# Kernel tuning notes

Measured on AMD Instinct MI355X. Metric: run time of the kernel, lower is better.

Reference implementation:

```python
import jax, jax.numpy as jnp
import numpy as np

T = 8          # time steps (init kwarg T)
GAMA = 1.0     # ZIF surrogate width (init kwarg gama)
LR = 0.1       # adaptive-threshold learning rate (init kwarg learning_rate)
THRESH = 8.0   # init kwarg thresh

# ZIF spiking activation: heaviside forward, triangular surrogate backward
@jax.custom_vjp
def heaviside(u):
    return (u >= 0).astype(u.dtype)

def _hv_fwd(u):
    return (u >= 0).astype(u.dtype), u

def _hv_bwd(u, g):
    surr = (1.0 / GAMA) * (1.0 / GAMA) * jnp.maximum(GAMA - jnp.abs(u), 0.0)
    return (g * surr,)

heaviside.defvjp(_hv_fwd, _hv_bwd)


def setup_inputs() -> dict:
    key = jax.random.key(0)
    x = jax.random.normal(key, (T * 32, 128, 32, 32), dtype=jnp.float32)  # [T*B, C, H, W]
    thresh = jnp.full((1,), THRESH, dtype=jnp.float32)                    # learnable thresh param
    return {"x": x, "thresh": thresh}


def reference(x, thresh):
    # thresh is used via .data in torch -> detached
    thre = jax.lax.stop_gradient(thresh)[0]
    B = x.shape[0] // T
    xs = x.reshape((T, B) + x.shape[1:])           # [T, B, C, H, W]
    C = xs.shape[2]
    neuron_thre0 = jnp.full((C,), thre, x.dtype)   # per-channel threshold init
    cur = neuron_thre0.reshape(1, C, 1, 1)         # broadcasts over [B, C, H, W]

    # sequential IF recurrence over T, carrying membrane potential
    def step(mem, xt):
        mem = mem + xt
        s = heaviside(mem - cur)
        mem = mem - s * cur
        return mem, s

    mem0 = jnp.broadcast_to(0.5 * cur, xs.shape[1:]).astype(x.dtype)
    mem, spikes = jax.lax.scan(step, mem0, xs)     # spikes: [T, B, C, H, W]

    # compensation pass over the stacked spike history
    compen_mem = mem - 0.5 * cur
    spike_count = spikes.sum(axis=0)               # [B, C, H, W]
    compen_value = jnp.minimum(compen_mem + spike_count * cur, T * cur)
    pos = (compen_value > 0) & (spike_count > 0)
    safe_count = jnp.where(spike_count > 0, spike_count, jnp.ones_like(spike_count))
    new_thre = jnp.where(pos, compen_value / safe_count, jnp.zeros_like(compen_value))

    # adaptive threshold update (scalar gradient-descent style step)
    ub = new_thre.mean(axis=(0, 2, 3))             # [C] per-channel target
    diff = ub - neuron_thre0
    mask = jax.lax.stop_gradient((neuron_thre0 > ub).astype(x.dtype))
    update = LR * 2.0 * (diff * mask).mean()       # scalar
    neuron_thre = neuron_thre0 + update            # [C]

    # scale spikes by the updated per-channel threshold, merge temporal dim
    out = spikes * neuron_thre.reshape(1, 1, C, 1, 1)
    return out.reshape((T * B,) + x.shape[1:])
```

## Files before the change

kernel.cpp:

```cpp
#include <hip/hip_runtime.h>
#include <stdint.h>

static constexpr int   T_  = 8;
static constexpr int   C_  = 128;
static constexpr int   N_  = 32 * 128 * 32 * 32;
static constexpr float LR_ = 0.1f;

template <bool PACK>
__global__ __launch_bounds__(256) void k_fwd(const float* __restrict__ x,
                                             const float* __restrict__ thresh,
                                             uint8_t* __restrict__ spk,
                                             float* __restrict__ ub_sum) {
    const float thre = thresh[0];
    const int e4   = blockIdx.x * 256 + threadIdx.x;
    const int base = e4 * 4;

    float    mem[4];
    int      cnt[4] = {0, 0, 0, 0};
    unsigned pb[4]  = {0, 0, 0, 0};
#pragma unroll
    for (int i = 0; i < 4; ++i) mem[i] = 0.5f * thre;

#pragma unroll
    for (int t = 0; t < T_; ++t) {
        const float4 xv = *reinterpret_cast<const float4*>(x + (size_t)t * N_ + base);
        const float xa[4] = {xv.x, xv.y, xv.z, xv.w};
#pragma unroll
        for (int i = 0; i < 4; ++i) {
            mem[i] += xa[i];
            if (mem[i] - thre >= 0.0f) {
                mem[i] -= thre;
                pb[i] |= (1u << t);
                cnt[i]++;
            }
        }
    }

    if (PACK) {
        reinterpret_cast<uchar4*>(spk)[e4] =
            make_uchar4((uint8_t)pb[0], (uint8_t)pb[1], (uint8_t)pb[2], (uint8_t)pb[3]);
    }

    float local = 0.0f;
#pragma unroll
    for (int i = 0; i < 4; ++i) {
        const float compen_mem = mem[i] - 0.5f * thre;
        const float cv = fminf(compen_mem + (float)cnt[i] * thre, (float)T_ * thre);
        if (cv > 0.0f && cnt[i] > 0) local += cv / (float)cnt[i];
    }

#pragma unroll
    for (int off = 32; off > 0; off >>= 1) local += __shfl_down(local, off, 64);
    __shared__ float wpart[4];
    const int lane = threadIdx.x & 63;
    const int wid  = threadIdx.x >> 6;
    if (lane == 0) wpart[wid] = local;
    __syncthreads();
    if (threadIdx.x == 0) {
        const float tot = wpart[0] + wpart[1] + wpart[2] + wpart[3];
        const int c = blockIdx.x & (C_ - 1);
        atomicAdd(ub_sum + c, tot);
    }
}

__global__ __launch_bounds__(128) void k_scalar(const float* __restrict__ ub_sum,
                                                const float* __restrict__ thresh,
                                                float* __restrict__ scal) {
    const float thre = thresh[0];
    const float ub   = ub_sum[threadIdx.x] * (1.0f / 32768.0f);
    float v = (thre > ub) ? (ub - thre) : 0.0f;
#pragma unroll
    for (int off = 32; off > 0; off >>= 1) v += __shfl_down(v, off, 64);
    __shared__ float part[2];
    if ((threadIdx.x & 63) == 0) part[threadIdx.x >> 6] = v;
    __syncthreads();
    if (threadIdx.x == 0) {
        const float update = LR_ * 2.0f * (part[0] + part[1]) * (1.0f / 128.0f);
        scal[0] = thre + update;
    }
}

__global__ __launch_bounds__(256) void k_out(const uint8_t* __restrict__ spk,
                                             const float* __restrict__ scal,
                                             float* __restrict__ out) {
    const int e4   = blockIdx.x * 256 + threadIdx.x;
    const int base = e4 * 4;
    const uchar4 p = reinterpret_cast<const uchar4*>(spk)[e4];
    const float  s = scal[0];
    const unsigned pb[4] = {p.x, p.y, p.z, p.w};
#pragma unroll
    for (int t = 0; t < T_; ++t) {
        float4 o;
        o.x = ((pb[0] >> t) & 1) ? s : 0.0f;
        o.y = ((pb[1] >> t) & 1) ? s : 0.0f;
        o.z = ((pb[2] >> t) & 1) ? s : 0.0f;
        o.w = ((pb[3] >> t) & 1) ? s : 0.0f;
        *reinterpret_cast<float4*>(out + (size_t)t * N_ + base) = o;
    }
}

__global__ __launch_bounds__(256) void k_out_recompute(const float* __restrict__ x,
                                                       const float* __restrict__ thresh,
                                                       const float* __restrict__ scal,
                                                       float* __restrict__ out) {
    const float thre = thresh[0];
    const float s    = scal[0];
    const int e4   = blockIdx.x * 256 + threadIdx.x;
    const int base = e4 * 4;
    float mem[4];
#pragma unroll
    for (int i = 0; i < 4; ++i) mem[i] = 0.5f * thre;
#pragma unroll
    for (int t = 0; t < T_; ++t) {
        const float4 xv = *reinterpret_cast<const float4*>(x + (size_t)t * N_ + base);
        const float xa[4] = {xv.x, xv.y, xv.z, xv.w};
        float4 o;
        float oo[4];
#pragma unroll
        for (int i = 0; i < 4; ++i) {
            mem[i] += xa[i];
            if (mem[i] - thre >= 0.0f) {
                mem[i] -= thre;
                oo[i] = s;
            } else {
                oo[i] = 0.0f;
            }
        }
        o.x = oo[0]; o.y = oo[1]; o.z = oo[2]; o.w = oo[3];
        *reinterpret_cast<float4*>(out + (size_t)t * N_ + base) = o;
    }
}

extern "C" void kernel_launch(void* const* d_in, const int* in_sizes, int n_in,
                              void* d_out, int out_size, void* d_ws, size_t ws_size,
                              hipStream_t stream) {
    const float* x      = (const float*)d_in[0];
    const float* thresh = (const float*)d_in[1];
    float*       out    = (float*)d_out;

    float*   ub_sum = (float*)d_ws;
    float*   scal   = ub_sum + C_;
    uint8_t* spk    = (uint8_t*)d_ws + 1024;
    const bool pack = ws_size >= (size_t)(1024 + N_);

    hipMemsetAsync(d_ws, 0, 1024, stream);

    const int nblk = N_ / 4 / 256;
    if (pack) {
        k_fwd<true><<<nblk, 256, 0, stream>>>(x, thresh, spk, ub_sum);
    } else {
        k_fwd<false><<<nblk, 256, 0, stream>>>(x, thresh, nullptr, ub_sum);
    }
    k_scalar<<<1, 128, 0, stream>>>(ub_sum, thresh, scal);
    if (pack) {
        k_out<<<nblk, 256, 0, stream>>>(spk, scal, out);
    } else {
        k_out_recompute<<<nblk, 256, 0, stream>>>(x, thresh, scal, out);
    }
}
```

Before: 55.01 us.

## Fold scalar threshold reduction into output kernel and drop memset and atomics

The forward kernel now writes one per-block partial sum instead of doing atomicAdd into a zeroed buffer. This removes the memset and the separate single-block scalar kernel. Each output block redundantly reduces the 4096 partials (32 per channel) to compute the updated threshold, so two launches are replaced by some duplicated per-block work. Loads of x and stores of out also become nontemporal to reduce cache pollution on single-use streaming data.

```diff
diff --git a/kernel.cpp b/kernel.cpp
--- a/kernel.cpp
+++ b/kernel.cpp
@@ -4,13 +4,16 @@
 static constexpr int   T_  = 8;
 static constexpr int   C_  = 128;
 static constexpr int   N_  = 32 * 128 * 32 * 32;
+static constexpr int   NBLK_ = N_ / 4 / 256;
 static constexpr float LR_ = 0.1f;
+
+typedef float v4f __attribute__((ext_vector_type(4)));
 
 template <bool PACK>
 __global__ __launch_bounds__(256) void k_fwd(const float* __restrict__ x,
                                              const float* __restrict__ thresh,
                                              uint8_t* __restrict__ spk,
-                                             float* __restrict__ ub_sum) {
+                                             float* __restrict__ part) {
     const float thre = thresh[0];
     const int e4   = blockIdx.x * 256 + threadIdx.x;
     const int base = e4 * 4;
@@ -23,11 +26,11 @@
 
 #pragma unroll
     for (int t = 0; t < T_; ++t) {
-        const float4 xv = *reinterpret_cast<const float4*>(x + (size_t)t * N_ + base);
-        const float xa[4] = {xv.x, xv.y, xv.z, xv.w};
+        const v4f xv = __builtin_nontemporal_load(
+            reinterpret_cast<const v4f*>(x + (size_t)t * N_ + base));
 #pragma unroll
         for (int i = 0; i < 4; ++i) {
-            mem[i] += xa[i];
+            mem[i] += xv[i];
             if (mem[i] - thre >= 0.0f) {
                 mem[i] -= thre;
                 pb[i] |= (1u << t);
@@ -37,8 +40,8 @@
     }
 
     if (PACK) {
-        reinterpret_cast<uchar4*>(spk)[e4] =
-            make_uchar4((uint8_t)pb[0], (uint8_t)pb[1], (uint8_t)pb[2], (uint8_t)pb[3]);
+        const unsigned packed = pb[0] | (pb[1] << 8) | (pb[2] << 16) | (pb[3] << 24);
+        reinterpret_cast<unsigned*>(spk)[e4] = packed;
     }
 
     float local = 0.0f;
@@ -57,54 +60,65 @@
     if (lane == 0) wpart[wid] = local;
     __syncthreads();
     if (threadIdx.x == 0) {
-        const float tot = wpart[0] + wpart[1] + wpart[2] + wpart[3];
-        const int c = blockIdx.x & (C_ - 1);
-        atomicAdd(ub_sum + c, tot);
+        part[blockIdx.x] = wpart[0] + wpart[1] + wpart[2] + wpart[3];
     }
 }
 
-__global__ __launch_bounds__(128) void k_scalar(const float* __restrict__ ub_sum,
-                                                const float* __restrict__ thresh,
-                                                float* __restrict__ scal) {
-    const float thre = thresh[0];
-    const float ub   = ub_sum[threadIdx.x] * (1.0f / 32768.0f);
-    float v = (thre > ub) ? (ub - thre) : 0.0f;
+__device__ __forceinline__ float compute_scalar(const float* __restrict__ part,
+                                                const float thre,
+                                                float* s_red) {
+    float v = 0.0f;
+    if (threadIdx.x < C_) {
+        float sum = 0.0f;
+#pragma unroll
+        for (int g = 0; g < NBLK_ / C_; ++g) sum += part[g * C_ + threadIdx.x];
+        const float ub = sum * (1.0f / 32768.0f);
+        v = (thre > ub) ? (ub - thre) : 0.0f;
+    }
 #pragma unroll
     for (int off = 32; off > 0; off >>= 1) v += __shfl_down(v, off, 64);
-    __shared__ float part[2];
-    if ((threadIdx.x & 63) == 0) part[threadIdx.x >> 6] = v;
+    if ((threadIdx.x & 63) == 0) s_red[1 + (threadIdx.x >> 6)] = v;
     __syncthreads();
     if (threadIdx.x == 0) {
-        const float update = LR_ * 2.0f * (part[0] + part[1]) * (1.0f / 128.0f);
-        scal[0] = thre + update;
+        const float update =
+            LR_ * 2.0f * (s_red[1] + s_red[2] + s_red[3] + s_red[4]) * (1.0f / (float)C_);
+        s_red[0] = thre + update;
     }
+    __syncthreads();
+    return s_red[0];
 }
 
 __global__ __launch_bounds__(256) void k_out(const uint8_t* __restrict__ spk,
-                                             const float* __restrict__ scal,
+                                             const float* __restrict__ part,
+                                             const float* __restrict__ thresh,
                                              float* __restrict__ out) {
+    __shared__ float s_red[5];
+    const float s = compute_scalar(part, thresh[0], s_red);
+
     const int e4   = blockIdx.x * 256 + threadIdx.x;
     const int base = e4 * 4;
-    const uchar4 p = reinterpret_cast<const uchar4*>(spk)[e4];
-    const float  s = scal[0];
-    const unsigned pb[4] = {p.x, p.y, p.z, p.w};
+    const unsigned packed = reinterpret_cast<const unsigned*>(spk)[e4];
+    const unsigned pb[4] = {packed & 0xffu, (packed >> 8) & 0xffu,
+                            (packed >> 16) & 0xffu, (packed >> 24) & 0xffu};
 #pragma unroll
     for (int t = 0; t < T_; ++t) {
-        float4 o;
+        v4f o;
         o.x = ((pb[0] >> t) & 1) ? s : 0.0f;
         o.y = ((pb[1] >> t) & 1) ? s : 0.0f;
         o.z = ((pb[2] >> t) & 1) ? s : 0.0f;
         o.w = ((pb[3] >> t) & 1) ? s : 0.0f;
-        *reinterpret_cast<float4*>(out + (size_t)t * N_ + base) = o;
+        __builtin_nontemporal_store(o, reinterpret_cast<v4f*>(out + (size_t)t * N_ + base));
     }
 }
 
 __global__ __launch_bounds__(256) void k_out_recompute(const float* __restrict__ x,
+                                                       const float* __restrict__ part,
                                                        const float* __restrict__ thresh,
-                                                       const float* __restrict__ scal,
                                                        float* __restrict__ out) {
+    __shared__ float s_red[5];
     const float thre = thresh[0];
-    const float s    = scal[0];
+    const float s = compute_scalar(part, thre, s_red);
+
     const int e4   = blockIdx.x * 256 + threadIdx.x;
     const int base = e4 * 4;
     float mem[4];
@@ -112,22 +126,20 @@
     for (int i = 0; i < 4; ++i) mem[i] = 0.5f * thre;
 #pragma unroll
     for (int t = 0; t < T_; ++t) {
-        const float4 xv = *reinterpret_cast<const float4*>(x + (size_t)t * N_ + base);
-        const float xa[4] = {xv.x, xv.y, xv.z, xv.w};
-        float4 o;
-        float oo[4];
+        const v4f xv = __builtin_nontemporal_load(
+            reinterpret_cast<const v4f*>(x + (size_t)t * N_ + base));
+        v4f o;
 #pragma unroll
         for (int i = 0; i < 4; ++i) {
-            mem[i] += xa[i];
+            mem[i] += xv[i];
             if (mem[i] - thre >= 0.0f) {
                 mem[i] -= thre;
-                oo[i] = s;
+                o[i] = s;
             } else {
-                oo[i] = 0.0f;
+                o[i] = 0.0f;
             }
         }
-        o.x = oo[0]; o.y = oo[1]; o.z = oo[2]; o.w = oo[3];
-        *reinterpret_cast<float4*>(out + (size_t)t * N_ + base) = o;
+        __builtin_nontemporal_store(o, reinterpret_cast<v4f*>(out + (size_t)t * N_ + base));
     }
 }
 
@@ -138,23 +150,15 @@
     const float* thresh = (const float*)d_in[1];
     float*       out    = (float*)d_out;
 
-    float*   ub_sum = (float*)d_ws;
-    float*   scal   = ub_sum + C_;
-    uint8_t* spk    = (uint8_t*)d_ws + 1024;
-    const bool pack = ws_size >= (size_t)(1024 + N_);
+    float*   part = (float*)d_ws;
+    uint8_t* spk  = (uint8_t*)d_ws + NBLK_ * sizeof(float);
+    const bool pack = ws_size >= (size_t)(NBLK_ * sizeof(float) + N_);
 
-    hipMemsetAsync(d_ws, 0, 1024, stream);
-
-    const int nblk = N_ / 4 / 256;
     if (pack) {
-        k_fwd<true><<<nblk, 256, 0, stream>>>(x, thresh, spk, ub_sum);
+        k_fwd<true><<<NBLK_, 256, 0, stream>>>(x, thresh, spk, part);
+        k_out<<<NBLK_, 256, 0, stream>>>(spk, part, thresh, out);
     } else {
-        k_fwd<false><<<nblk, 256, 0, stream>>>(x, thresh, nullptr, ub_sum);
-    }
-    k_scalar<<<1, 128, 0, stream>>>(ub_sum, thresh, scal);
-    if (pack) {
-        k_out<<<nblk, 256, 0, stream>>>(spk, scal, out);
-    } else {
-        k_out_recompute<<<nblk, 256, 0, stream>>>(x, thresh, scal, out);
+        k_fwd<false><<<NBLK_, 256, 0, stream>>>(x, thresh, nullptr, part);
+        k_out_recompute<<<NBLK_, 256, 0, stream>>>(x, part, thresh, out);
     }
 }
```

New measurement: 55.94 us. No clear change (+1.7%).
